# Kernel optimization log

Hardware: AMD Instinct MI355X
Metric: run time of the kernel (lower is better)

## Reference

```python
import jax, jax.numpy as jnp
import numpy as np
import math

G, T, D, B = 20000, 1536, 512, 256
TOPK = 32


def setup_inputs() -> dict:
    key = jax.random.key(0)
    k1, k2, k3, k4 = jax.random.split(key, 4)
    tg_dec = jax.random.normal(k1, (G, D), dtype=jnp.float32)
    tf_base = jax.random.normal(k2, (T, D), dtype=jnp.float32)
    tf_expr = jax.random.normal(k3, (B, T), dtype=jnp.float32)
    motif_mask = jax.random.randint(k4, (G, T), 0, 2).astype(jnp.int32)
    scale = jnp.full((1,), 0.1, dtype=jnp.float32)  # nn.Parameter scale
    return {"tg_dec": tg_dec, "tf_base": tf_base, "tf_expr": tf_expr,
            "motif_mask": motif_mask, "scale": scale}


def reference(tg_dec, tf_base, tf_expr, motif_mask, scale):
    # scaled similarity: [G, T]
    sim = jnp.matmul(tg_dec, tf_base.T) / math.sqrt(tf_base.shape[1])
    # masked fill where motif prior is absent
    sim = jnp.where(motif_mask == 0, -jnp.inf, sim)
    attn = jax.nn.softmax(sim, axis=-1)
    attn = jnp.nan_to_num(attn, nan=0.0)
    # top-k selection + scatter mask + renormalize
    _, topk_idx = jax.lax.top_k(attn, TOPK)              # [G, TOPK]
    rows = jnp.arange(attn.shape[0])[:, None]
    mask = jnp.zeros_like(attn).at[rows, topk_idx].set(1.0)
    attn = attn * mask
    attn = attn / (attn.sum(axis=-1, keepdims=True) + 1e-8)
    # weighted combine: [B, G]
    tf_scalar = jnp.matmul(tf_expr, attn.T)
    # dropout is identity in eval mode
    return (scale[0] * tf_scalar, attn)
```

## Files before the change

### kernel.cpp

```cpp
#include <hip/hip_runtime.h>
#include <cstdint>

typedef unsigned short u16;
typedef unsigned int   u32;
typedef unsigned long long u64;

#define G_ROWS 20000
#define G_PAD  20096
#define T_DIM  1536
#define D_DIM  512
#define B_DIM  256
#define TOPK   32
#define SIM_SCALE 0.04419417382415922f
#define SQRT_D    22.62741699796952f
#define BOUND_EPS 2.0e-4f

typedef __bf16 bf16x8 __attribute__((ext_vector_type(8)));
typedef float  f32x4  __attribute__((ext_vector_type(4)));

__device__ __forceinline__ u16 f2bf(float f) {
  u32 u = __float_as_uint(f);
  u += 0x7fffu + ((u >> 16) & 1u);
  return (u16)(u >> 16);
}
__device__ __forceinline__ float bf2f(u16 h) {
  return __uint_as_float(((u32)h) << 16);
}
__device__ __forceinline__ u32 fkey(float v) {
  u32 b = __float_as_uint(v);
  return (b & 0x80000000u) ? ~b : (b | 0x80000000u);
}
__device__ __forceinline__ float funkey(u32 o) {
  u32 b = (o & 0x80000000u) ? (o & 0x7FFFFFFFu) : ~o;
  return __uint_as_float(b);
}

__global__ __launch_bounds__(256) void prep(const float* __restrict__ tg_dec,
                                            const float* __restrict__ tf_base,
                                            const float* __restrict__ tf_expr,
                                            u16* __restrict__ Ah, u16* __restrict__ Al,
                                            u16* __restrict__ Bh, u16* __restrict__ Bl,
                                            float* __restrict__ tfT)
{
  __shared__ float tile[32][33];
  const int b = blockIdx.x;
  const int tid = threadIdx.x;
  if (b < 10816) {
    const float* src; u16 *hi, *lo; int valid_rows; int bb;
    if (b < 10048) { src = tg_dec; hi = Ah; lo = Al; valid_rows = G_ROWS; bb = b; }
    else           { src = tf_base; hi = Bh; lo = Bl; valid_rows = T_DIM; bb = b - 10048; }
    size_t i = ((size_t)bb * 256 + tid) * 4;
    int row = (int)(i >> 9);
    float4 a = make_float4(0.f, 0.f, 0.f, 0.f);
    if (row < valid_rows) a = *(const float4*)(src + i);
    float v[4] = {a.x, a.y, a.z, a.w};
    u16 h[4], l[4];
#pragma unroll
    for (int c = 0; c < 4; ++c) {
      h[c] = f2bf(v[c]);
      l[c] = f2bf(v[c] - bf2f(h[c]));
    }
    *(uint2*)(hi + i) = make_uint2((u32)h[0] | ((u32)h[1] << 16), (u32)h[2] | ((u32)h[3] << 16));
    *(uint2*)(lo + i) = make_uint2((u32)l[0] | ((u32)l[1] << 16), (u32)l[2] | ((u32)l[3] << 16));
  } else {
    const int t = b - 10816;
    const int x = tid & 31, y = tid >> 5;
    const int bt = (t % 48) * 32;
    const int bb = (t / 48) * 32;
#pragma unroll
    for (int i = 0; i < 32; i += 8) tile[y + i][x] = tf_expr[(size_t)(bb + y + i) * T_DIM + bt + x];
    __syncthreads();
#pragma unroll
    for (int i = 0; i < 32; i += 8) tfT[(size_t)(bt + y + i) * B_DIM + bb + x] = tile[x][y + i];
  }
}

__device__ __forceinline__ void gl16(const u16* g, u16* l) {
  __builtin_amdgcn_global_load_lds((__attribute__((address_space(1))) void*)(void*)g,
                                   (__attribute__((address_space(3))) void*)l, 16, 0, 0);
}

#define NBX 6
#define NWG 474

__global__ __launch_bounds__(512, 2) void gemm_split(const u16* __restrict__ Ah, const u16* __restrict__ Al,
                                                     const u16* __restrict__ Bh, const u16* __restrict__ Bl,
                                                     float* __restrict__ Sim)
{
  __shared__ u16 sm[65536];

  const int orig = blockIdx.x;
  const int xcd  = orig & 7;
  const int q    = NWG >> 3, r = NWG & 7;
  const int wgid = (xcd < r ? xcd * (q + 1) : r * (q + 1) + (xcd - r) * q) + (orig >> 3);
  const int by   = wgid / NBX;
  const int bx   = wgid - by * NBX;
  const int bm0  = by * 256;
  const int bn0  = bx * 256;

  const int tid  = threadIdx.x;
  const int lane = tid & 63;
  const int wv   = tid >> 6;
  const int wm   = wv >> 2;
  const int wn   = wv & 3;
  const int la8  = lane << 3;

  const int sub  = wv << 1;
  const int srow = lane & 15;
  const int skc  = (lane >> 4) << 3;
  const u16* gA0 = Ah + (size_t)(bm0 + (sub + 0) * 16 + srow) * 512 + skc;
  const u16* gA1 = Ah + (size_t)(bm0 + (sub + 1) * 16 + srow) * 512 + skc;
  const u16* gAl0 = Al + (size_t)(bm0 + (sub + 0) * 16 + srow) * 512 + skc;
  const u16* gAl1 = Al + (size_t)(bm0 + (sub + 1) * 16 + srow) * 512 + skc;
  const u16* gB0 = Bh + (size_t)(bn0 + (sub + 0) * 16 + srow) * 512 + skc;
  const u16* gB1 = Bh + (size_t)(bn0 + (sub + 1) * 16 + srow) * 512 + skc;
  const u16* gBl0 = Bl + (size_t)(bn0 + (sub + 0) * 16 + srow) * 512 + skc;
  const u16* gBl1 = Bl + (size_t)(bn0 + (sub + 1) * 16 + srow) * 512 + skc;

#define STAGE_A(p, ktn) do {                                   \
    const size_t ko = (size_t)(ktn) << 5;                      \
    u16* d = sm + (p) * 16384 + sub * 512;                     \
    gl16(gA0 + ko,  d);                                        \
    gl16(gA1 + ko,  d + 512);                                  \
    gl16(gAl0 + ko, d + 8192);                                 \
    gl16(gAl1 + ko, d + 8192 + 512);                           \
  } while (0)
#define STAGE_B(p, ktn) do {                                   \
    const size_t ko = (size_t)(ktn) << 5;                      \
    u16* d = sm + 32768 + (p) * 16384 + sub * 512;             \
    gl16(gB0 + ko,  d);                                        \
    gl16(gB1 + ko,  d + 512);                                  \
    gl16(gBl0 + ko, d + 8192);                                 \
    gl16(gBl1 + ko, d + 8192 + 512);                           \
  } while (0)

  f32x4 acc[8][4];
#pragma unroll
  for (int i = 0; i < 8; ++i)
#pragma unroll
    for (int j = 0; j < 4; ++j) acc[i][j] = (f32x4){0.f, 0.f, 0.f, 0.f};

  bf16x8 aH[4], aL[4], bH[4], bL[4];

#define READ_A(rbA, half) do {                                                     \
    _Pragma("unroll")                                                              \
    for (int i = 0; i < 4; ++i) {                                                  \
      aH[i] = *(const bf16x8*)((rbA) + (wm * 8 + (half) * 4 + i) * 512 + la8);     \
      aL[i] = *(const bf16x8*)((rbA) + 8192 + (wm * 8 + (half) * 4 + i) * 512 + la8); \
    }                                                                              \
  } while (0)
#define READ_B(rbB, half) do {                                                     \
    _Pragma("unroll")                                                              \
    for (int i = 0; i < 2; ++i) {                                                  \
      bH[(half) * 2 + i] = *(const bf16x8*)((rbB) + (wn * 4 + (half) * 2 + i) * 512 + la8); \
      bL[(half) * 2 + i] = *(const bf16x8*)((rbB) + 8192 + (wn * 4 + (half) * 2 + i) * 512 + la8); \
    }                                                                              \
  } while (0)
#define MFMA_Q(qm, qn) do {                                                        \
    __builtin_amdgcn_s_setprio(1);                                                 \
    _Pragma("unroll")                                                              \
    for (int m2 = 0; m2 < 4; ++m2)                                                 \
      _Pragma("unroll")                                                            \
      for (int n2 = 0; n2 < 2; ++n2) {                                             \
        const int mi = (qm) * 4 + m2, ni = (qn) * 2 + n2;                          \
        acc[mi][ni] = __builtin_amdgcn_mfma_f32_16x16x32_bf16(aH[m2], bH[ni], acc[mi][ni], 0, 0, 0); \
        acc[mi][ni] = __builtin_amdgcn_mfma_f32_16x16x32_bf16(aH[m2], bL[ni], acc[mi][ni], 0, 0, 0); \
        acc[mi][ni] = __builtin_amdgcn_mfma_f32_16x16x32_bf16(aL[m2], bH[ni], acc[mi][ni], 0, 0, 0); \
      }                                                                            \
    __builtin_amdgcn_s_setprio(0);                                                 \
  } while (0)
#define LGKM0 do { asm volatile("s_waitcnt lgkmcnt(0)" ::: "memory"); __builtin_amdgcn_sched_barrier(0); } while (0)
#define BAR   do { __builtin_amdgcn_sched_barrier(0); __builtin_amdgcn_s_barrier(); } while (0)

  STAGE_A(0, 0);
  STAGE_B(0, 0);
  STAGE_A(1, 1);

#pragma unroll 2
  for (int kt = 0; kt < 16; ++kt) {
    const u16* rbA = sm + (kt & 1) * 16384;
    const u16* rbB = sm + 32768 + (kt & 1) * 16384;

    asm volatile("s_waitcnt vmcnt(4)" ::: "memory");
    BAR;
    READ_A(rbA, 0);
    READ_B(rbB, 0);
    LGKM0;
    MFMA_Q(0, 0);
    BAR;

    if (kt < 15) STAGE_B((kt + 1) & 1, kt + 1);
    READ_B(rbB, 1);
    LGKM0;
    MFMA_Q(0, 1);
    BAR;

    READ_A(rbA, 1);
    LGKM0;
    MFMA_Q(1, 0);
    BAR;

    if (kt < 14) STAGE_A(kt & 1, kt + 2);
    MFMA_Q(1, 1);
  }
#undef STAGE_A
#undef STAGE_B
#undef READ_A
#undef READ_B
#undef MFMA_Q
#undef LGKM0
#undef BAR

  const int erow0 = bm0 + (wm << 7) + ((lane >> 4) << 2);
  const int ecol0 = bn0 + (wn << 6) + (lane & 15);
#pragma unroll
  for (int mi = 0; mi < 8; ++mi)
#pragma unroll
    for (int rr = 0; rr < 4; ++rr) {
      int row = erow0 + mi * 16 + rr;
      if (row < G_ROWS) {
#pragma unroll
        for (int ni = 0; ni < 4; ++ni)
          Sim[(size_t)row * T_DIM + ecol0 + ni * 16] = acc[mi][ni][rr] * SIM_SCALE;
      }
    }
}

__device__ __forceinline__ int count_ge(const float* v, float tau) {
  int c = 0;
#pragma unroll
  for (int j = 0; j < 24; ++j) c += (int)__popcll(__ballot(v[j] >= tau));
  return c;
}
__device__ __forceinline__ u64 bitonic64_desc(u64 key, int lane) {
#pragma unroll
  for (int k = 2; k <= 64; k <<= 1) {
#pragma unroll
    for (int j = k >> 1; j > 0; j >>= 1) {
      u64 p = __shfl_xor(key, j, 64);
      bool lower = (lane & j) == 0;
      bool asc   = (lane & k) != 0;
      u64 mn = (key < p) ? key : p;
      u64 mx = (key < p) ? p : key;
      key = (lower == asc) ? mn : mx;
    }
  }
  return key;
}

__global__ __launch_bounds__(256) void topk_kernel(float* __restrict__ Sim, const int* __restrict__ mask,
                                                   const float* __restrict__ tg_dec,
                                                   const float* __restrict__ tf_base,
                                                   int* __restrict__ tIdx, float* __restrict__ tW)
{
  __shared__ u32 cval[4][64];
  __shared__ int cidxs[4][64];
  const int lane = threadIdx.x & 63;
  const int wv   = threadIdx.x >> 6;
  const int g    = blockIdx.x * 4 + wv;
  float* row = Sim + (size_t)g * T_DIM;
  const int* mrow = mask + (size_t)g * T_DIM;

  float v[24];
#pragma unroll
  for (int j = 0; j < 6; ++j) {
    float4 q = *(const float4*)(row + j * 256 + lane * 4);
    int4  mq = *(const int4*)(mrow + j * 256 + lane * 4);
    v[j * 4 + 0] = mq.x ? q.x : -INFINITY;
    v[j * 4 + 1] = mq.y ? q.y : -INFINITY;
    v[j * 4 + 2] = mq.z ? q.z : -INFINITY;
    v[j * 4 + 3] = mq.w ? q.w : -INFINITY;
  }

  const float TH0 = 1.25f, TH1 = 1.40f, TH2 = 1.55f, TH3 = 1.70f, TH4 = 1.85f, TH5 = 2.00f;
  int n0 = 0, n1 = 0, n2 = 0, n3 = 0, n4 = 0, n5 = 0, nv = 0;
#pragma unroll
  for (int j = 0; j < 24; ++j) {
    float x = v[j];
    n0 += (x >= TH0); n1 += (x >= TH1); n2 += (x >= TH2);
    n3 += (x >= TH3); n4 += (x >= TH4); n5 += (x >= TH5);
    nv += (x != -INFINITY);
  }
  u64 p0 = (u64)(u32)n0 | ((u64)(u32)n1 << 16) | ((u64)(u32)n2 << 32) | ((u64)(u32)n3 << 48);
  u64 p1 = (u64)(u32)n4 | ((u64)(u32)n5 << 16) | ((u64)(u32)nv << 32);
#pragma unroll
  for (int off = 32; off > 0; off >>= 1) {
    p0 += __shfl_xor(p0, off, 64);
    p1 += __shfl_xor(p1, off, 64);
  }
  int c[6];
  c[0] = (int)(p0 & 0xFFFF); c[1] = (int)((p0 >> 16) & 0xFFFF);
  c[2] = (int)((p0 >> 32) & 0xFFFF); c[3] = (int)((p0 >> 48) & 0xFFFF);
  c[4] = (int)(p1 & 0xFFFF); c[5] = (int)((p1 >> 16) & 0xFFFF);
  const int cvalid = (int)((p1 >> 32) & 0xFFFF);

  float tau; int cnt;
  if (cvalid <= 64) { tau = -3.0e38f; cnt = cvalid; }
  else {
    int is = -1;
#pragma unroll
    for (int i = 0; i < 6; ++i) if (c[i] >= 33) is = i;
    const float THv[7] = {TH0, TH1, TH2, TH3, TH4, TH5, 8.0f};
    if (is >= 0 && c[is] <= 64) { tau = THv[is]; cnt = c[is]; }
    else {
      float lo, hi;
      if (is < 0) { lo = -4.0f; hi = TH0; }
      else        { lo = THv[is]; hi = THv[is + 1]; }
      tau = lo; cnt = 1000;
      for (int it = 0; it < 16; ++it) {
        float mid = 0.5f * (lo + hi);
        int cm = count_ge(v, mid);
        if (cm > 64)      lo = mid;
        else if (cm < 33) hi = mid;
        else { tau = mid; cnt = cm; break; }
      }
      if (cnt == 1000) tau = lo;
    }
  }

  int base = 0;
#pragma unroll
  for (int j = 0; j < 24; ++j) {
    bool pred = (v[j] >= tau);
    u64 bmc = __ballot(pred);
    int pos = base + (int)__popcll(bmc & ((1ull << lane) - 1ull));
    int idx = (j >> 2) * 256 + lane * 4 + (j & 3);
    if (pred && pos < 64) { cval[wv][pos] = fkey(v[j]); cidxs[wv][pos] = idx; }
    base += (int)__popcll(bmc);
  }
  const int cnt_eff = (base < 64) ? base : 64;

  u64 key = 0;
  if (lane < cnt_eff)
    key = ((u64)cval[wv][lane] << 32) | (u64)(u32)(~(u32)cidxs[wv][lane]);

  key = bitonic64_desc(key, lane);
  int   myidx = (int)(~(u32)key);
  float myv   = (key != 0) ? funkey((u32)(key >> 32)) : -INFINITY;

  float v31 = __shfl(myv, 31, 64);
  float v32 = __shfl(myv, 32, 64);
  if (cnt_eff > TOPK && (v31 - v32) < 2.0f * BOUND_EPS) {
    bool flag = (lane < cnt_eff) &&
                (myv >= v32 - 2.0f * BOUND_EPS) && (myv <= v31 + 2.0f * BOUND_EPS);
    if (flag) {
      const float* arow_g = tg_dec + (size_t)g * D_DIM;
      const float* brow   = tf_base + (size_t)myidx * D_DIM;
      float s1 = 0.f, s2 = 0.f;
#pragma unroll 8
      for (int k = 0; k < 384; k += 4) {
        float4 av = *(const float4*)(arow_g + k);
        float4 bv = *(const float4*)(brow + k);
        s1 = fmaf(av.x, bv.x, s1); s1 = fmaf(av.y, bv.y, s1);
        s1 = fmaf(av.z, bv.z, s1); s1 = fmaf(av.w, bv.w, s1);
      }
#pragma unroll 8
      for (int k = 384; k < 512; k += 4) {
        float4 av = *(const float4*)(arow_g + k);
        float4 bv = *(const float4*)(brow + k);
        s2 = fmaf(av.x, bv.x, s2); s2 = fmaf(av.y, bv.y, s2);
        s2 = fmaf(av.z, bv.z, s2); s2 = fmaf(av.w, bv.w, s2);
      }
      myv = (s1 + s2) / SQRT_D;
      key = ((u64)fkey(myv) << 32) | (u64)(u32)(~(u32)myidx);
    }
    key = bitonic64_desc(key, lane);
    myidx = (int)(~(u32)key);
    myv   = (key != 0) ? funkey((u32)(key >> 32)) : -INFINITY;
  }

  const bool selme = (lane < TOPK) && (lane < cnt_eff);
  float mx = __shfl(myv, 0, 64);
  float e = selme ? __expf(myv - mx) : 0.f;
  float E = e;
#pragma unroll
  for (int off = 32; off > 0; off >>= 1) E += __shfl_xor(E, off, 64);
  float rden = (E > 0.f) ? (1.f / E) : 0.f;
  float w = e * rden;

  const float4 z4 = make_float4(0.f, 0.f, 0.f, 0.f);
#pragma unroll
  for (int j = 0; j < 6; ++j) *(float4*)(row + j * 256 + lane * 4) = z4;
  asm volatile("s_waitcnt vmcnt(0)" ::: "memory");
  if (selme) row[myidx] = w;

  if (cnt_eff < TOPK && lane >= cnt_eff && lane < TOPK) {
    tIdx[(size_t)g * TOPK + lane] = 0; tW[(size_t)g * TOPK + lane] = 0.f;
  }
  if (selme) {
    tIdx[(size_t)g * TOPK + lane] = myidx;
    tW[(size_t)g * TOPK + lane]   = w;
  }
}

__global__ __launch_bounds__(256) void combine_kernel(const float* __restrict__ tfT, const int* __restrict__ tIdx,
                                                      const float* __restrict__ tW, const float* __restrict__ scalep,
                                                      float* __restrict__ out0)
{
  __shared__ int   sIdx[16 * 32];
  __shared__ float sW[16 * 32];
  const int tid = threadIdx.x;
  const int g0 = blockIdx.x * 16;
  for (int i = tid; i < 512; i += 256) {
    sIdx[i] = tIdx[(size_t)g0 * 32 + i];
    sW[i]   = tW[(size_t)g0 * 32 + i];
  }
  __syncthreads();
  const float scale = scalep[0];
  float acc[16];
#pragma unroll
  for (int gi = 0; gi < 16; ++gi) acc[gi] = 0.f;
#pragma unroll 4
  for (int gi = 0; gi < 16; ++gi) {
    float a = 0.f;
#pragma unroll
    for (int k = 0; k < 32; ++k) {
      float w = sW[gi * 32 + k];
      int t   = sIdx[gi * 32 + k];
      a += w * tfT[(size_t)t * B_DIM + tid];
    }
    acc[gi] = a;
  }
  float* dst = out0 + (size_t)tid * G_ROWS + g0;
#pragma unroll
  for (int q = 0; q < 4; ++q) {
    float4 o = make_float4(scale * acc[4*q], scale * acc[4*q+1], scale * acc[4*q+2], scale * acc[4*q+3]);
    *(float4*)(dst + 4 * q) = o;
  }
}

extern "C" void kernel_launch(void* const* d_in, const int* in_sizes, int n_in,
                              void* d_out, int out_size, void* d_ws, size_t ws_size,
                              hipStream_t stream)
{
  const float* tg_dec     = (const float*)d_in[0];
  const float* tf_base    = (const float*)d_in[1];
  const float* tf_expr    = (const float*)d_in[2];
  const int*   motif_mask = (const int*)d_in[3];
  const float* scale      = (const float*)d_in[4];

  float* out0 = (float*)d_out;
  float* attn = out0 + (size_t)B_DIM * G_ROWS;

  char* ws = (char*)d_ws;
  u16*   Ah    = (u16*)(ws);
  u16*   Al    = (u16*)(ws + 20578304);
  u16*   Bh    = (u16*)(ws + 41156608);
  u16*   Bl    = (u16*)(ws + 42729472);
  float* tfT   = (float*)(ws + 44302336);
  int*   tIdx  = (int*)(ws + 45875200);
  float* tW    = (float*)(ws + 48435200);

  prep<<<11200, 256, 0, stream>>>(tg_dec, tf_base, tf_expr, Ah, Al, Bh, Bl, tfT);
  gemm_split<<<NWG, 512, 0, stream>>>(Ah, Al, Bh, Bl, attn);
  topk_kernel<<<5000, 256, 0, stream>>>(attn, motif_mask, tg_dec, tf_base, tIdx, tW);
  combine_kernel<<<1250, 256, 0, stream>>>(tfT, tIdx, tW, scale, out0);
}
```

Baseline: 425.0 us.

## Fuse mask into GEMM epilogue, loosen GEMM barriers, vectorize combine gathers

Applies the motif mask in the GEMM epilogue by writing -inf directly into Sim, so the top-k kernel no longer reads the mask. Removes most per-quarter barriers and lgkmcnt waits in the GEMM main loop, issues the next B stage earlier, and confines setprio to the final MFMA quarter. Restructures the combine kernel so each wave handles four rows with float4 gathers over the B dimension. The looser synchronization relies on compiler-inserted waits for LDS reads and risks overwriting buffers still being read; the mask-in-epilogue adds strided int loads to the GEMM.

```diff
diff --git a/kernel.cpp b/kernel.cpp
--- a/kernel.cpp
+++ b/kernel.cpp
@@ -85,6 +85,7 @@
 
 __global__ __launch_bounds__(512, 2) void gemm_split(const u16* __restrict__ Ah, const u16* __restrict__ Al,
                                                      const u16* __restrict__ Bh, const u16* __restrict__ Bl,
+                                                     const int* __restrict__ Mask,
                                                      float* __restrict__ Sim)
 {
   __shared__ u16 sm[65536];
@@ -108,12 +109,12 @@
   const int sub  = wv << 1;
   const int srow = lane & 15;
   const int skc  = (lane >> 4) << 3;
-  const u16* gA0 = Ah + (size_t)(bm0 + (sub + 0) * 16 + srow) * 512 + skc;
-  const u16* gA1 = Ah + (size_t)(bm0 + (sub + 1) * 16 + srow) * 512 + skc;
+  const u16* gA0  = Ah + (size_t)(bm0 + (sub + 0) * 16 + srow) * 512 + skc;
+  const u16* gA1  = Ah + (size_t)(bm0 + (sub + 1) * 16 + srow) * 512 + skc;
   const u16* gAl0 = Al + (size_t)(bm0 + (sub + 0) * 16 + srow) * 512 + skc;
   const u16* gAl1 = Al + (size_t)(bm0 + (sub + 1) * 16 + srow) * 512 + skc;
-  const u16* gB0 = Bh + (size_t)(bn0 + (sub + 0) * 16 + srow) * 512 + skc;
-  const u16* gB1 = Bh + (size_t)(bn0 + (sub + 1) * 16 + srow) * 512 + skc;
+  const u16* gB0  = Bh + (size_t)(bn0 + (sub + 0) * 16 + srow) * 512 + skc;
+  const u16* gB1  = Bh + (size_t)(bn0 + (sub + 1) * 16 + srow) * 512 + skc;
   const u16* gBl0 = Bl + (size_t)(bn0 + (sub + 0) * 16 + srow) * 512 + skc;
   const u16* gBl1 = Bl + (size_t)(bn0 + (sub + 1) * 16 + srow) * 512 + skc;
 
@@ -157,7 +158,6 @@
     }                                                                              \
   } while (0)
 #define MFMA_Q(qm, qn) do {                                                        \
-    __builtin_amdgcn_s_setprio(1);                                                 \
     _Pragma("unroll")                                                              \
     for (int m2 = 0; m2 < 4; ++m2)                                                 \
       _Pragma("unroll")                                                            \
@@ -167,10 +167,8 @@
         acc[mi][ni] = __builtin_amdgcn_mfma_f32_16x16x32_bf16(aH[m2], bL[ni], acc[mi][ni], 0, 0, 0); \
         acc[mi][ni] = __builtin_amdgcn_mfma_f32_16x16x32_bf16(aL[m2], bH[ni], acc[mi][ni], 0, 0, 0); \
       }                                                                            \
-    __builtin_amdgcn_s_setprio(0);                                                 \
   } while (0)
-#define LGKM0 do { asm volatile("s_waitcnt lgkmcnt(0)" ::: "memory"); __builtin_amdgcn_sched_barrier(0); } while (0)
-#define BAR   do { __builtin_amdgcn_sched_barrier(0); __builtin_amdgcn_s_barrier(); } while (0)
+#define SBAR do { __builtin_amdgcn_sched_barrier(0); __builtin_amdgcn_s_barrier(); __builtin_amdgcn_sched_barrier(0); } while (0)
 
   STAGE_A(0, 0);
   STAGE_B(0, 0);
@@ -181,36 +179,33 @@
     const u16* rbA = sm + (kt & 1) * 16384;
     const u16* rbB = sm + 32768 + (kt & 1) * 16384;
 
-    asm volatile("s_waitcnt vmcnt(4)" ::: "memory");
-    BAR;
+    if (kt < 15) asm volatile("s_waitcnt vmcnt(4)" ::: "memory");
+    else         asm volatile("s_waitcnt vmcnt(0)" ::: "memory");
+    SBAR;
+
     READ_A(rbA, 0);
     READ_B(rbB, 0);
-    LGKM0;
+    if (kt < 15) STAGE_B((kt + 1) & 1, kt + 1);
     MFMA_Q(0, 0);
-    BAR;
-
-    if (kt < 15) STAGE_B((kt + 1) & 1, kt + 1);
     READ_B(rbB, 1);
-    LGKM0;
     MFMA_Q(0, 1);
-    BAR;
-
     READ_A(rbA, 1);
-    LGKM0;
     MFMA_Q(1, 0);
-    BAR;
-
+
+    SBAR;
     if (kt < 14) STAGE_A(kt & 1, kt + 2);
+    __builtin_amdgcn_s_setprio(1);
     MFMA_Q(1, 1);
+    __builtin_amdgcn_s_setprio(0);
   }
 #undef STAGE_A
 #undef STAGE_B
 #undef READ_A
 #undef READ_B
 #undef MFMA_Q
-#undef LGKM0
-#undef BAR
-
+#undef SBAR
+
+  const float NEG_INF = __uint_as_float(0xff800000u);
   const int erow0 = bm0 + (wm << 7) + ((lane >> 4) << 2);
   const int ecol0 = bn0 + (wn << 6) + (lane & 15);
 #pragma unroll
@@ -219,9 +214,13 @@
     for (int rr = 0; rr < 4; ++rr) {
       int row = erow0 + mi * 16 + rr;
       if (row < G_ROWS) {
-#pragma unroll
-        for (int ni = 0; ni < 4; ++ni)
-          Sim[(size_t)row * T_DIM + ecol0 + ni * 16] = acc[mi][ni][rr] * SIM_SCALE;
+        const int* mrow = Mask + (size_t)row * T_DIM + ecol0;
+        float*     srow = Sim  + (size_t)row * T_DIM + ecol0;
+#pragma unroll
+        for (int ni = 0; ni < 4; ++ni) {
+          int m = mrow[ni * 16];
+          srow[ni * 16] = m ? acc[mi][ni][rr] * SIM_SCALE : NEG_INF;
+        }
       }
     }
 }
@@ -248,7 +247,7 @@
   return key;
 }
 
-__global__ __launch_bounds__(256) void topk_kernel(float* __restrict__ Sim, const int* __restrict__ mask,
+__global__ __launch_bounds__(256) void topk_kernel(float* __restrict__ Sim,
                                                    const float* __restrict__ tg_dec,
                                                    const float* __restrict__ tf_base,
                                                    int* __restrict__ tIdx, float* __restrict__ tW)
@@ -259,17 +258,12 @@
   const int wv   = threadIdx.x >> 6;
   const int g    = blockIdx.x * 4 + wv;
   float* row = Sim + (size_t)g * T_DIM;
-  const int* mrow = mask + (size_t)g * T_DIM;
 
   float v[24];
 #pragma unroll
   for (int j = 0; j < 6; ++j) {
     float4 q = *(const float4*)(row + j * 256 + lane * 4);
-    int4  mq = *(const int4*)(mrow + j * 256 + lane * 4);
-    v[j * 4 + 0] = mq.x ? q.x : -INFINITY;
-    v[j * 4 + 1] = mq.y ? q.y : -INFINITY;
-    v[j * 4 + 2] = mq.z ? q.z : -INFINITY;
-    v[j * 4 + 3] = mq.w ? q.w : -INFINITY;
+    v[j * 4 + 0] = q.x; v[j * 4 + 1] = q.y; v[j * 4 + 2] = q.z; v[j * 4 + 3] = q.w;
   }
 
   const float TH0 = 1.25f, TH1 = 1.40f, TH2 = 1.55f, TH3 = 1.70f, TH4 = 1.85f, TH5 = 2.00f;
@@ -399,33 +393,40 @@
 {
   __shared__ int   sIdx[16 * 32];
   __shared__ float sW[16 * 32];
-  const int tid = threadIdx.x;
-  const int g0 = blockIdx.x * 16;
+  const int tid  = threadIdx.x;
+  const int lane = tid & 63;
+  const int wv   = tid >> 6;
+  const int g0   = blockIdx.x * 16;
   for (int i = tid; i < 512; i += 256) {
     sIdx[i] = tIdx[(size_t)g0 * 32 + i];
     sW[i]   = tW[(size_t)g0 * 32 + i];
   }
   __syncthreads();
   const float scale = scalep[0];
-  float acc[16];
-#pragma unroll
-  for (int gi = 0; gi < 16; ++gi) acc[gi] = 0.f;
+  const int gl = wv << 2;
+  float acc[4][4];
+#pragma unroll
+  for (int gi = 0; gi < 4; ++gi)
+#pragma unroll
+    for (int c = 0; c < 4; ++c) acc[gi][c] = 0.f;
+
 #pragma unroll 4
-  for (int gi = 0; gi < 16; ++gi) {
-    float a = 0.f;
-#pragma unroll
-    for (int k = 0; k < 32; ++k) {
-      float w = sW[gi * 32 + k];
-      int t   = sIdx[gi * 32 + k];
-      a += w * tfT[(size_t)t * B_DIM + tid];
-    }
-    acc[gi] = a;
-  }
-  float* dst = out0 + (size_t)tid * G_ROWS + g0;
-#pragma unroll
-  for (int q = 0; q < 4; ++q) {
-    float4 o = make_float4(scale * acc[4*q], scale * acc[4*q+1], scale * acc[4*q+2], scale * acc[4*q+3]);
-    *(float4*)(dst + 4 * q) = o;
+  for (int k = 0; k < 32; ++k) {
+#pragma unroll
+    for (int gi = 0; gi < 4; ++gi) {
+      int   t = sIdx[(gl + gi) * 32 + k];
+      float w = sW[(gl + gi) * 32 + k];
+      float4 vv = *(const float4*)(tfT + (size_t)t * B_DIM + lane * 4);
+      acc[gi][0] = fmaf(w, vv.x, acc[gi][0]);
+      acc[gi][1] = fmaf(w, vv.y, acc[gi][1]);
+      acc[gi][2] = fmaf(w, vv.z, acc[gi][2]);
+      acc[gi][3] = fmaf(w, vv.w, acc[gi][3]);
+    }
+  }
+#pragma unroll
+  for (int c = 0; c < 4; ++c) {
+    float4 o = make_float4(scale * acc[0][c], scale * acc[1][c], scale * acc[2][c], scale * acc[3][c]);
+    *(float4*)(out0 + (size_t)(lane * 4 + c) * G_ROWS + g0 + gl) = o;
   }
 }
 
@@ -452,7 +453,7 @@
   float* tW    = (float*)(ws + 48435200);
 
   prep<<<11200, 256, 0, stream>>>(tg_dec, tf_base, tf_expr, Ah, Al, Bh, Bl, tfT);
-  gemm_split<<<NWG, 512, 0, stream>>>(Ah, Al, Bh, Bl, attn);
-  topk_kernel<<<5000, 256, 0, stream>>>(attn, motif_mask, tg_dec, tf_base, tIdx, tW);
+  gemm_split<<<NWG, 512, 0, stream>>>(Ah, Al, Bh, Bl, motif_mask, attn);
+  topk_kernel<<<5000, 256, 0, stream>>>(attn, tg_dec, tf_base, tIdx, tW);
   combine_kernel<<<1250, 256, 0, stream>>>(tfT, tIdx, tW, scale, out0);
 }
```

Result: slower. 440.8 us (+3.7%).
